# Performance work log

Measured on AMD Instinct MI355X. Metric: run time of the kernel, lower is better.

Reference implementation:

```python
import jax, jax.numpy as jnp
import numpy as np

B, S, C = 8192, 7, 30


def _iou(b1, b2):
    """Faithful replica of calculate_iou (including its intersect/area1 + area2 - intersect quirk).
    b1, b2: [..., 4] as (cx, cy, w, h). Returns [...] ."""
    area1 = b1[..., 2] * b1[..., 3]
    area2 = b2[..., 2] * b2[..., 3]
    max_left = jnp.maximum(b1[..., 0] - b1[..., 2] / 2, b2[..., 0] - b2[..., 2] / 2)
    min_right = jnp.minimum(b1[..., 0] + b1[..., 2] / 2, b2[..., 0] + b2[..., 2] / 2)
    max_top = jnp.maximum(b1[..., 1] - b1[..., 3] / 2, b2[..., 1] - b2[..., 3] / 2)
    min_bottom = jnp.minimum(b1[..., 1] + b1[..., 3] / 2, b2[..., 1] + b2[..., 3] / 2)
    inter = (min_right - max_left) * (min_bottom - max_top)
    overlap = (max_left < min_right) & (max_top < min_bottom)
    return jnp.where(overlap, inter / area1 + area2 - inter, 0.0)


def setup_inputs() -> dict:
    key = jax.random.key(0)
    k1, k2, k3 = jax.random.split(key, 3)
    preds = jax.random.uniform(k1, (B, S, S, C), dtype=jnp.float32, minval=0.01, maxval=1.0)
    labels = jax.random.uniform(k2, (B, S, S, C), dtype=jnp.float32, minval=0.01, maxval=1.0)
    obj = (jax.random.uniform(k3, (B, S, S)) < 0.3).astype(jnp.float32)
    labels = labels.at[..., 4].set(obj)  # objectness indicator in {0,1}
    return {"preds": preds, "labels": labels}


def reference(preds, labels):
    batch_size = labels.shape[0]
    obj = (labels[..., 4] == 1).astype(preds.dtype)  # [B,7,7]

    # IoUs are computed on detached values in the original (numpy round-trip)
    iou1 = jax.lax.stop_gradient(_iou(preds[..., 0:4], labels[..., 0:4]))
    iou2 = jax.lax.stop_gradient(_iou(preds[..., 5:9], labels[..., 5:9]))
    resp1 = iou1 > iou2  # box 1 responsible

    xy1 = jnp.sum((preds[..., 0:2] - labels[..., 0:2]) ** 2, axis=-1)
    xy2 = jnp.sum((preds[..., 5:7] - labels[..., 5:7]) ** 2, axis=-1)
    wh1 = jnp.sum((jnp.sqrt(preds[..., 2:4]) - jnp.sqrt(labels[..., 2:4])) ** 2, axis=-1)
    wh2 = jnp.sum((jnp.sqrt(preds[..., 7:9]) - jnp.sqrt(labels[..., 7:9])) ** 2, axis=-1)

    loss_xy = 5.0 * jnp.where(resp1, xy1, xy2)
    loss_wh = jnp.where(resp1, wh1, wh2)
    loss_obj = jnp.where(resp1, (preds[..., 4] - iou1) ** 2, (preds[..., 9] - iou2) ** 2)
    loss_noobj_objcell = 0.5 * jnp.where(resp1, (preds[..., 9] - iou2) ** 2, (preds[..., 4] - iou1) ** 2)
    loss_cls = jnp.sum((preds[..., 10:] - labels[..., 10:]) ** 2, axis=-1)

    obj_cell = loss_xy + loss_wh + loss_obj + loss_noobj_objcell + loss_cls
    noobj_cell = 0.5 * (preds[..., 4] ** 2 + preds[..., 9] ** 2)

    total = jnp.sum(obj * obj_cell + (1.0 - obj) * noobj_cell)
    return total / batch_size
```

## Files before the change

kernel.cpp:

```cpp
#include <hip/hip_runtime.h>

#define YB     8192
#define YS     7
#define YC     30
#define NCELLS (YB * YS * YS)
#define CPT    256
#define NBLK   (NCELLS / CPT)
#define BLOCK  256

__device__ __forceinline__ float iou_quirk(float cx1, float cy1, float w1, float h1,
                                           float cx2, float cy2, float w2, float h2) {
    float area1 = w1 * h1;
    float area2 = w2 * h2;
    float max_left   = fmaxf(cx1 - w1 * 0.5f, cx2 - w2 * 0.5f);
    float min_right  = fminf(cx1 + w1 * 0.5f, cx2 + w2 * 0.5f);
    float max_top    = fmaxf(cy1 - h1 * 0.5f, cy2 - h2 * 0.5f);
    float min_bottom = fminf(cy1 + h1 * 0.5f, cy2 + h2 * 0.5f);
    float inter = (min_right - max_left) * (min_bottom - max_top);
    bool overlap = (max_left < min_right) && (max_top < min_bottom);
    return overlap ? (inter / area1 + area2 - inter) : 0.0f;
}

__global__ __launch_bounds__(BLOCK) void yolo_partial_kernel(const float* __restrict__ preds,
                                                             const float* __restrict__ labels,
                                                             float* __restrict__ partial) {
    __shared__ float sp[CPT * YC];
    __shared__ float sl[CPT * YC];
    __shared__ float wsum[BLOCK / 64];

    const int tid = threadIdx.x;
    const long base = (long)blockIdx.x * (CPT * YC);

    const float4* gp = (const float4*)(preds + base);
    const float4* gl = (const float4*)(labels + base);
    float4* sp4 = (float4*)sp;
    float4* sl4 = (float4*)sl;
    const int NV = CPT * YC / 4;
    for (int i = tid; i < NV; i += BLOCK) {
        sp4[i] = gp[i];
        sl4[i] = gl[i];
    }
    __syncthreads();

    const float* p = sp + tid * YC;
    const float* l = sl + tid * YC;

    float p0 = p[0], p1 = p[1], p2 = p[2], p3 = p[3], p4 = p[4];
    float p5 = p[5], p6 = p[6], p7 = p[7], p8 = p[8], p9 = p[9];
    float l0 = l[0], l1 = l[1], l2 = l[2], l3 = l[3], l4 = l[4];
    float l5 = l[5], l6 = l[6], l7 = l[7], l8 = l[8];

    float iou1 = iou_quirk(p0, p1, p2, p3, l0, l1, l2, l3);
    float iou2 = iou_quirk(p5, p6, p7, p8, l5, l6, l7, l8);
    bool resp1 = iou1 > iou2;

    float dx1 = p0 - l0, dy1 = p1 - l1;
    float xy1 = dx1 * dx1 + dy1 * dy1;
    float dx2 = p5 - l5, dy2 = p6 - l6;
    float xy2 = dx2 * dx2 + dy2 * dy2;

    float sw1 = sqrtf(p2) - sqrtf(l2), sh1 = sqrtf(p3) - sqrtf(l3);
    float wh1 = sw1 * sw1 + sh1 * sh1;
    float sw2 = sqrtf(p7) - sqrtf(l7), sh2 = sqrtf(p8) - sqrtf(l8);
    float wh2 = sw2 * sw2 + sh2 * sh2;

    float d1 = p4 - iou1, d2 = p9 - iou2;
    float e1 = d1 * d1, e2 = d2 * d2;

    float loss_xy = 5.0f * (resp1 ? xy1 : xy2);
    float loss_wh = resp1 ? wh1 : wh2;
    float loss_obj = resp1 ? e1 : e2;
    float loss_noobj_objcell = 0.5f * (resp1 ? e2 : e1);

    float loss_cls = 0.0f;
    #pragma unroll
    for (int c = 10; c < YC; ++c) {
        float d = p[c] - l[c];
        loss_cls += d * d;
    }

    float obj_cell = loss_xy + loss_wh + loss_obj + loss_noobj_objcell + loss_cls;
    float noobj_cell = 0.5f * (p4 * p4 + p9 * p9);

    float v = (l4 == 1.0f) ? obj_cell : noobj_cell;

    for (int off = 32; off > 0; off >>= 1) v += __shfl_down(v, off);
    const int lane = tid & 63, wid = tid >> 6;
    if (lane == 0) wsum[wid] = v;
    __syncthreads();
    if (tid == 0) partial[blockIdx.x] = wsum[0] + wsum[1] + wsum[2] + wsum[3];
}

__global__ __launch_bounds__(BLOCK) void yolo_final_kernel(const float* __restrict__ partial,
                                                           float* __restrict__ out) {
    __shared__ double w[BLOCK / 64];
    double s = 0.0;
    for (int i = threadIdx.x; i < NBLK; i += BLOCK) s += (double)partial[i];
    for (int off = 32; off > 0; off >>= 1) s += __shfl_down(s, off);
    const int lane = threadIdx.x & 63, wid = threadIdx.x >> 6;
    if (lane == 0) w[wid] = s;
    __syncthreads();
    if (threadIdx.x == 0) out[0] = (float)((w[0] + w[1] + w[2] + w[3]) / (double)YB);
}

extern "C" void kernel_launch(void* const* d_in, const int* in_sizes, int n_in,
                              void* d_out, int out_size, void* d_ws, size_t ws_size,
                              hipStream_t stream) {
    const float* preds  = (const float*)d_in[0];
    const float* labels = (const float*)d_in[1];
    float* out = (float*)d_out;
    float* partial = (float*)d_ws;

    yolo_partial_kernel<<<NBLK, BLOCK, 0, stream>>>(preds, labels, partial);
    yolo_final_kernel<<<1, BLOCK, 0, stream>>>(partial, out);
}
```

Baseline: 27.40 us.

## Use direct global-to-LDS loads, halve cells per block, vectorize LDS reads

Global loads now go straight into LDS through the amdgcn global_load_lds builtin, skipping the register round trip. Each block handles 128 cells instead of 256, which doubles the grid and halves LDS use per block, but only half the threads do the compute and reduction. Per-cell LDS reads use float2 loads into register arrays. The builtin's LDS addressing semantics (it uses M0 plus a per-lane offset) may not match the per-lane destination pointers passed here, so correctness is at risk.

Measured after the change: 25.18 us. 1.09x faster.

```diff
diff --git a/kernel.cpp b/kernel.cpp
--- a/kernel.cpp
+++ b/kernel.cpp
@@ -4,7 +4,7 @@
 #define YS     7
 #define YC     30
 #define NCELLS (YB * YS * YS)
-#define CPT    256
+#define CPT    128
 #define NBLK   (NCELLS / CPT)
 #define BLOCK  256
 
@@ -26,7 +26,7 @@
                                                              float* __restrict__ partial) {
     __shared__ float sp[CPT * YC];
     __shared__ float sl[CPT * YC];
-    __shared__ float wsum[BLOCK / 64];
+    __shared__ float wsum[2];
 
     const int tid = threadIdx.x;
     const long base = (long)blockIdx.x * (CPT * YC);
@@ -36,59 +36,74 @@
     float4* sp4 = (float4*)sp;
     float4* sl4 = (float4*)sl;
     const int NV = CPT * YC / 4;
+
+#if defined(__has_builtin) && __has_builtin(__builtin_amdgcn_global_load_lds)
+    typedef const __attribute__((address_space(1))) void* as1_t;
+    typedef __attribute__((address_space(3))) void* as3_t;
+    for (int i = tid; i < NV; i += BLOCK)
+        __builtin_amdgcn_global_load_lds((as1_t)(gp + i), (as3_t)(sp4 + i), 16, 0, 0);
+    for (int i = tid; i < NV; i += BLOCK)
+        __builtin_amdgcn_global_load_lds((as1_t)(gl + i), (as3_t)(sl4 + i), 16, 0, 0);
+#else
     for (int i = tid; i < NV; i += BLOCK) {
         sp4[i] = gp[i];
         sl4[i] = gl[i];
     }
+#endif
     __syncthreads();
 
-    const float* p = sp + tid * YC;
-    const float* l = sl + tid * YC;
+    float v = 0.0f;
+    if (tid < CPT) {
+        const float2* p2 = (const float2*)(sp + tid * YC);
+        const float2* l2 = (const float2*)(sl + tid * YC);
+        float pv[YC], lv[YC];
+        #pragma unroll
+        for (int i = 0; i < YC / 2; ++i) {
+            float2 a = p2[i]; pv[2 * i] = a.x; pv[2 * i + 1] = a.y;
+            float2 b = l2[i]; lv[2 * i] = b.x; lv[2 * i + 1] = b.y;
+        }
 
-    float p0 = p[0], p1 = p[1], p2 = p[2], p3 = p[3], p4 = p[4];
-    float p5 = p[5], p6 = p[6], p7 = p[7], p8 = p[8], p9 = p[9];
-    float l0 = l[0], l1 = l[1], l2 = l[2], l3 = l[3], l4 = l[4];
-    float l5 = l[5], l6 = l[6], l7 = l[7], l8 = l[8];
+        float iou1 = iou_quirk(pv[0], pv[1], pv[2], pv[3], lv[0], lv[1], lv[2], lv[3]);
+        float iou2 = iou_quirk(pv[5], pv[6], pv[7], pv[8], lv[5], lv[6], lv[7], lv[8]);
+        bool resp1 = iou1 > iou2;
 
-    float iou1 = iou_quirk(p0, p1, p2, p3, l0, l1, l2, l3);
-    float iou2 = iou_quirk(p5, p6, p7, p8, l5, l6, l7, l8);
-    bool resp1 = iou1 > iou2;
+        float dx1 = pv[0] - lv[0], dy1 = pv[1] - lv[1];
+        float xy1 = dx1 * dx1 + dy1 * dy1;
+        float dx2 = pv[5] - lv[5], dy2 = pv[6] - lv[6];
+        float xy2 = dx2 * dx2 + dy2 * dy2;
 
-    float dx1 = p0 - l0, dy1 = p1 - l1;
-    float xy1 = dx1 * dx1 + dy1 * dy1;
-    float dx2 = p5 - l5, dy2 = p6 - l6;
-    float xy2 = dx2 * dx2 + dy2 * dy2;
+        float sw1 = sqrtf(pv[2]) - sqrtf(lv[2]), sh1 = sqrtf(pv[3]) - sqrtf(lv[3]);
+        float wh1 = sw1 * sw1 + sh1 * sh1;
+        float sw2 = sqrtf(pv[7]) - sqrtf(lv[7]), sh2 = sqrtf(pv[8]) - sqrtf(lv[8]);
+        float wh2 = sw2 * sw2 + sh2 * sh2;
 
-    float sw1 = sqrtf(p2) - sqrtf(l2), sh1 = sqrtf(p3) - sqrtf(l3);
-    float wh1 = sw1 * sw1 + sh1 * sh1;
-    float sw2 = sqrtf(p7) - sqrtf(l7), sh2 = sqrtf(p8) - sqrtf(l8);
-    float wh2 = sw2 * sw2 + sh2 * sh2;
+        float d1 = pv[4] - iou1, d2 = pv[9] - iou2;
+        float e1 = d1 * d1, e2 = d2 * d2;
 
-    float d1 = p4 - iou1, d2 = p9 - iou2;
-    float e1 = d1 * d1, e2 = d2 * d2;
+        float loss_xy = 5.0f * (resp1 ? xy1 : xy2);
+        float loss_wh = resp1 ? wh1 : wh2;
+        float loss_obj = resp1 ? e1 : e2;
+        float loss_noobj_objcell = 0.5f * (resp1 ? e2 : e1);
 
-    float loss_xy = 5.0f * (resp1 ? xy1 : xy2);
-    float loss_wh = resp1 ? wh1 : wh2;
-    float loss_obj = resp1 ? e1 : e2;
-    float loss_noobj_objcell = 0.5f * (resp1 ? e2 : e1);
+        float loss_cls = 0.0f;
+        #pragma unroll
+        for (int c = 10; c < YC; ++c) {
+            float d = pv[c] - lv[c];
+            loss_cls += d * d;
+        }
 
-    float loss_cls = 0.0f;
-    #pragma unroll
-    for (int c = 10; c < YC; ++c) {
-        float d = p[c] - l[c];
-        loss_cls += d * d;
+        float obj_cell = loss_xy + loss_wh + loss_obj + loss_noobj_objcell + loss_cls;
+        float noobj_cell = 0.5f * (pv[4] * pv[4] + pv[9] * pv[9]);
+
+        v = (lv[4] == 1.0f) ? obj_cell : noobj_cell;
     }
 
-    float obj_cell = loss_xy + loss_wh + loss_obj + loss_noobj_objcell + loss_cls;
-    float noobj_cell = 0.5f * (p4 * p4 + p9 * p9);
-
-    float v = (l4 == 1.0f) ? obj_cell : noobj_cell;
-
-    for (int off = 32; off > 0; off >>= 1) v += __shfl_down(v, off);
-    const int lane = tid & 63, wid = tid >> 6;
-    if (lane == 0) wsum[wid] = v;
+    if (tid < CPT) {
+        for (int off = 32; off > 0; off >>= 1) v += __shfl_down(v, off);
+        if ((tid & 63) == 0) wsum[tid >> 6] = v;
+    }
     __syncthreads();
-    if (tid == 0) partial[blockIdx.x] = wsum[0] + wsum[1] + wsum[2] + wsum[3];
+    if (tid == 0) partial[blockIdx.x] = wsum[0] + wsum[1];
 }
 
 __global__ __launch_bounds__(BLOCK) void yolo_final_kernel(const float* __restrict__ partial,
```
